# Kernel tuning notes

Measured on AMD Instinct MI355X. Metric: run time of the kernel, lower is better.

Reference implementation:

```python
import jax, jax.numpy as jnp
import numpy as np

DIAG_PENALTY = 100.0

def setup_inputs() -> dict:
    key = jax.random.key(0)
    x = jax.random.normal(key, (8192, 768), dtype=jnp.float32)
    return {"x": x, "coef": 1.0, "tau": 1.0}

def _similarity(x):
    # sim[i, j] = -||x_i - x_j||^2, computed via GEMM expansion
    # ||a - b||^2 = ||a||^2 + ||b||^2 - 2 a.b  (avoids the (N,N,D) intermediate)
    sq = jnp.sum(x * x, axis=1)                      # [N]
    gram = x @ x.T                                   # [N, N]
    sim = 2.0 * gram - sq[:, None] - sq[None, :]     # = -||x_i - x_j||^2
    n = x.shape[0]
    sim = sim - DIAG_PENALTY * jnp.eye(n, dtype=x.dtype)
    return sim

def reference(x, coef, tau):
    sim = _similarity(x) * tau                       # [N, N]
    logp = jax.nn.log_softmax(sim, axis=-1)          # stable, single pass
    prob = jnp.exp(logp)
    entropy = -jnp.sum(prob * logp, axis=-1)         # [N]
    return coef * jnp.mean(entropy)
```

## Files before the change

kernel.cpp:

```cpp
#include <hip/hip_runtime.h>
#include <hip/hip_bf16.h>
#include <hip/hip_fp8.h>
#include <cstdint>
#include <cstddef>

#define GN 8192
#define GD 768
#define NB 64
#define NTILE 2080
#define KI 12

#define LOG2E 1.4426950408889634f
#define LN2 0.6931471805599453f

typedef __attribute__((ext_vector_type(4))) float f32x4;
typedef __attribute__((ext_vector_type(2))) long l64x2;

typedef __attribute__((address_space(1))) const unsigned int gu32;
typedef __attribute__((address_space(3))) unsigned int lu32;

__device__ __forceinline__ void gl2lds16(const void* g, void* l) {
    __builtin_amdgcn_global_load_lds((gu32*)g, (lu32*)l, 16, 0, 0);
}

__device__ __forceinline__ float hexp2(float x) {
    return __builtin_amdgcn_exp2f(x);
}

template <int CTRL>
__device__ __forceinline__ float fdpp(float x) {
    return __int_as_float(__builtin_amdgcn_update_dpp(
        0, __float_as_int(x), CTRL, 0xF, 0xF, true));
}
__device__ __forceinline__ float qmax16(float v) {
    v = fmaxf(v, fdpp<0x128>(v));
    v = fmaxf(v, fdpp<0x124>(v));
    v = fmaxf(v, fdpp<0x122>(v));
    v = fmaxf(v, fdpp<0x121>(v));
    return v;
}
__device__ __forceinline__ float qsum16(float v) {
    v += fdpp<0x128>(v);
    v += fdpp<0x124>(v);
    v += fdpp<0x122>(v);
    v += fdpp<0x121>(v);
    return v;
}

__device__ __forceinline__ int swz(int r, int q) {
    return ((r >> 1) << 7) + (((((r & 1) << 2) | q) ^ ((r >> 1) & 7)) << 4);
}

__global__ __launch_bounds__(256) void prep_kernel(const float* __restrict__ x,
                                                   unsigned char* __restrict__ xq,
                                                   float* __restrict__ sq,
                                                   float* __restrict__ out) {
    if (blockIdx.x == 0 && threadIdx.x == 0) out[0] = 0.f;
    const int w = threadIdx.x >> 6, lane = threadIdx.x & 63;
    const int row = blockIdx.x * 4 + w;
    const float4* xr = (const float4*)(x + (size_t)row * GD);
    unsigned int* xqr = (unsigned int*)(xq + (size_t)row * GD);
    float s = 0.f;
#pragma unroll
    for (int i = 0; i < 3; ++i) {
        float4 v = xr[lane + 64 * i];
        __hip_fp8_e4m3 q0(v.x), q1(v.y), q2(v.z), q3(v.w);
        float d0 = (float)q0, d1 = (float)q1, d2 = (float)q2, d3 = (float)q3;
        s += d0 * d0 + d1 * d1 + d2 * d2 + d3 * d3;
        xqr[lane + 64 * i] = (unsigned int)q0.__x | ((unsigned int)q1.__x << 8) |
                             ((unsigned int)q2.__x << 16) | ((unsigned int)q3.__x << 24);
    }
#pragma unroll
    for (int off = 1; off < 64; off <<= 1) s += __shfl_xor(s, off);
    if (lane == 0) sq[row] = s;
}

__global__ __launch_bounds__(256, 4) void sym_gemm_entropy(
    const unsigned char* __restrict__ xq, const float* __restrict__ sq,
    const float* __restrict__ taup, float* __restrict__ pm,
    float* __restrict__ ps, float* __restrict__ pt) {
    __shared__ __align__(16) char lds[32768];
    float (*tmrg)[4][3] = (float (*)[4][3])lds;

    const int tid = threadIdx.x;
    const int lane = tid & 63;
    const int w = tid >> 6;
    const int quad = lane >> 4, cl = lane & 15;

    const int b = blockIdx.x;
    int I = (int)((sqrtf(8.0f * (float)b + 1.0f) - 1.0f) * 0.5f);
    while ((I + 1) * (I + 2) / 2 <= b) ++I;
    while (I * (I + 1) / 2 > b) --I;
    const int J = b - I * (I + 1) / 2;
    const int row_base = I * 128;
    const int col_base = J * 128;
    const float taub = (*taup) * LOG2E;

    const int bb = (tid & 7) ^ ((tid >> 3) & 7);
    const int sRow = ((tid >> 3) << 1) | (bb >> 2);
    const int sKb = (bb & 3) * 16;
    const unsigned char* gA = xq + (size_t)(row_base + sRow) * GD + sKb;
    const unsigned char* gB = xq + (size_t)(col_base + sRow) * GD + sKb;

    int offA[2], offB[8];
#pragma unroll
    for (int ti = 0; ti < 2; ++ti) offA[ti] = swz(w * 32 + ti * 16 + cl, quad);
#pragma unroll
    for (int tj = 0; tj < 8; ++tj) offB[tj] = swz(tj * 16 + cl, quad);

    f32x4 acc[2][8];
#pragma unroll
    for (int i = 0; i < 2; ++i)
#pragma unroll
        for (int j = 0; j < 8; ++j) acc[i][j] = (f32x4){0.f, 0.f, 0.f, 0.f};

    gl2lds16(gA, lds + tid * 16);
    gl2lds16(gA + (size_t)64 * GD, lds + 4096 + tid * 16);
    gl2lds16(gB, lds + 8192 + tid * 16);
    gl2lds16(gB + (size_t)64 * GD, lds + 12288 + tid * 16);

#pragma unroll 2
    for (int kk = 0; kk < KI; ++kk) {
        __syncthreads();

        const char* Ab = lds + (kk & 1) * 16384;
        const char* Bb = Ab + 8192;
        l64x2 aF[2], bF[8];
#pragma unroll
        for (int ti = 0; ti < 2; ++ti) aF[ti] = *(const l64x2*)(Ab + offA[ti]);
#pragma unroll
        for (int tj = 0; tj < 8; ++tj) bF[tj] = *(const l64x2*)(Bb + offB[tj]);

        if (kk + 1 < KI) {
            char* An = lds + ((kk + 1) & 1) * 16384;
            const int ko = (kk + 1) * 64;
            gl2lds16(gA + ko, An + tid * 16);
            gl2lds16(gA + (size_t)64 * GD + ko, An + 4096 + tid * 16);
            gl2lds16(gB + ko, An + 8192 + tid * 16);
            gl2lds16(gB + (size_t)64 * GD + ko, An + 12288 + tid * 16);
        }

#pragma unroll
        for (int ti = 0; ti < 2; ++ti)
#pragma unroll
            for (int tj = 0; tj < 8; ++tj) {
                acc[ti][tj] = __builtin_amdgcn_mfma_f32_16x16x32_fp8_fp8(
                    aF[ti].x, bF[tj].x, acc[ti][tj], 0, 0, 0);
                acc[ti][tj] = __builtin_amdgcn_mfma_f32_16x16x32_fp8_fp8(
                    aF[ti].y, bF[tj].y, acc[ti][tj], 0, 0, 0);
            }
    }

    const float t2 = 2.f * taub;
    const float pen = 100.f * taub;
    float ar[8];
    int rowg[8];
#pragma unroll
    for (int ti = 0; ti < 2; ++ti)
#pragma unroll
        for (int rg = 0; rg < 4; ++rg) {
            int r = row_base + w * 32 + ti * 16 + quad * 4 + rg;
            rowg[ti * 4 + rg] = r;
            ar[ti * 4 + rg] = -taub * sq[r];
        }
    float ac[8];
#pragma unroll
    for (int tj = 0; tj < 8; ++tj) ac[tj] = -taub * sq[col_base + tj * 16 + cl];

    float* pmJ = pm + (size_t)J * GN;
    float* psJ = ps + (size_t)J * GN;
    float* ptJ = pt + (size_t)J * GN;

#pragma unroll
    for (int ti = 0; ti < 2; ++ti)
#pragma unroll
        for (int rg = 0; rg < 4; ++rg) {
            const int idx = ti * 4 + rg;
            float uu[8];
            float mloc = -1e30f;
            if (I == J) {
#pragma unroll
                for (int tj = 0; tj < 8; ++tj) {
                    float u = fmaf(t2, acc[ti][tj][rg], ac[tj]);
                    if (rowg[idx] == col_base + tj * 16 + cl) u -= pen;
                    uu[tj] = u;
                    mloc = fmaxf(mloc, u);
                }
            } else {
#pragma unroll
                for (int tj = 0; tj < 8; ++tj) {
                    float u = fmaf(t2, acc[ti][tj][rg], ac[tj]);
                    uu[tj] = u;
                    mloc = fmaxf(mloc, u);
                }
            }
            mloc = qmax16(mloc);
            float s = 0.f, t = 0.f;
#pragma unroll
            for (int tj = 0; tj < 8; ++tj) {
                float d = uu[tj] - mloc;
                float e = hexp2(d);
                s += e;
                t += e * d;
            }
            s = qsum16(s);
            t = qsum16(t);
            if (cl == 0) {
                int r = rowg[idx];
                pmJ[r] = mloc + ar[idx];
                psJ[r] = s;
                ptJ[r] = t;
            }
        }

    if (I != J) {
        __syncthreads();
#pragma unroll
        for (int tj = 0; tj < 8; ++tj) {
            float uu[8];
            float mloc = -1e30f;
#pragma unroll
            for (int ti = 0; ti < 2; ++ti)
#pragma unroll
                for (int rg = 0; rg < 4; ++rg) {
                    float u = fmaf(t2, acc[ti][tj][rg], ar[ti * 4 + rg]);
                    uu[ti * 4 + rg] = u;
                    mloc = fmaxf(mloc, u);
                }
            mloc = fmaxf(mloc, __shfl_xor(mloc, 16));
            mloc = fmaxf(mloc, __shfl_xor(mloc, 32));
            float s = 0.f, t = 0.f;
#pragma unroll
            for (int k = 0; k < 8; ++k) {
                float d = uu[k] - mloc;
                float e = hexp2(d);
                s += e;
                t += e * d;
            }
            s += __shfl_xor(s, 16);
            t += __shfl_xor(t, 16);
            s += __shfl_xor(s, 32);
            t += __shfl_xor(t, 32);
            if (quad == 0) {
                int c = tj * 16 + cl;
                tmrg[c][w][0] = mloc + ac[tj];
                tmrg[c][w][1] = s;
                tmrg[c][w][2] = t;
            }
        }
        __syncthreads();
        if (tid < 128) {
            float m = tmrg[tid][0][0], S = tmrg[tid][0][1], T = tmrg[tid][0][2];
#pragma unroll
            for (int ww = 1; ww < 4; ++ww) {
                float mc = tmrg[tid][ww][0], Sc = tmrg[tid][ww][1], Tc = tmrg[tid][ww][2];
                float mn = fmaxf(m, mc);
                float ea = hexp2(m - mn), eb = hexp2(mc - mn);
                T = (T + (m - mn) * S) * ea + (Tc + (mc - mn) * Sc) * eb;
                S = S * ea + Sc * eb;
                m = mn;
            }
            int c = col_base + tid;
            pm[(size_t)I * GN + c] = m;
            ps[(size_t)I * GN + c] = S;
            pt[(size_t)I * GN + c] = T;
        }
    }
}

__global__ __launch_bounds__(256) void combine(const float* __restrict__ pm,
                                               const float* __restrict__ ps,
                                               const float* __restrict__ pt,
                                               const float* __restrict__ coefp,
                                               float* __restrict__ out) {
    const int t = threadIdx.x;
    const int r = t & 63;
    const int chunk = t >> 6;
    const int row = blockIdx.x * 64 + r;
    float m = -1e30f, S = 0.f, T = 0.f;
#pragma unroll
    for (int i = 0; i < 16; ++i) {
        const int c = chunk * 16 + i;
        float mc = pm[(size_t)c * GN + row];
        float Sc = ps[(size_t)c * GN + row];
        float Tc = pt[(size_t)c * GN + row];
        float mn = fmaxf(m, mc);
        float ea = __builtin_amdgcn_exp2f(m - mn), eb = __builtin_amdgcn_exp2f(mc - mn);
        T = (T + (m - mn) * S) * ea + (Tc + (mc - mn) * Sc) * eb;
        S = S * ea + Sc * eb;
        m = mn;
    }
    __shared__ float lm[4][64], lS[4][64], lT[4][64];
    lm[chunk][r] = m;
    lS[chunk][r] = S;
    lT[chunk][r] = T;
    __syncthreads();
    if (t < 64) {
        float M = lm[0][r], Sa = lS[0][r], Ta = lT[0][r];
#pragma unroll
        for (int cc = 1; cc < 4; ++cc) {
            float mc = lm[cc][r], Sc = lS[cc][r], Tc = lT[cc][r];
            float mn = fmaxf(M, mc);
            float ea = __builtin_amdgcn_exp2f(M - mn), eb = __builtin_amdgcn_exp2f(mc - mn);
            Ta = (Ta + (M - mn) * Sa) * ea + (Tc + (mc - mn) * Sc) * eb;
            Sa = Sa * ea + Sc * eb;
            M = mn;
        }
        float ent2 = __log2f(Sa) - Ta / Sa;
#pragma unroll
        for (int off = 1; off < 64; off <<= 1) ent2 += __shfl_xor(ent2, off);
        if (t == 0) atomicAdd(out, ent2 * coefp[0] * (LN2 / (float)GN));
    }
}

extern "C" void kernel_launch(void* const* d_in, const int* in_sizes, int n_in,
                              void* d_out, int out_size, void* d_ws, size_t ws_size,
                              hipStream_t stream) {
    const float* x = (const float*)d_in[0];
    const float* coefp = (const float*)d_in[1];
    const float* taup = (const float*)d_in[2];
    float* out = (float*)d_out;

    char* ws = (char*)d_ws;
    unsigned char* xq = (unsigned char*)ws;
    float* sq = (float*)(ws + 6291456);
    float* pm = (float*)(ws + 6324224);
    float* ps = (float*)(ws + 6324224 + 2097152);
    float* pt = (float*)(ws + 6324224 + 2 * 2097152);

    prep_kernel<<<GN / 4, 256, 0, stream>>>(x, xq, sq, out);
    sym_gemm_entropy<<<NTILE, 256, 0, stream>>>(xq, sq, taup, pm, ps, pt);
    combine<<<GN / 64, 256, 0, stream>>>(pm, ps, pt, coefp, out);
}
```

Baseline: 128.7 us.

## Switch fp8 GEMM to 32x32x64 scaled MFMA and rework fragment layout

Replaces the 16x16x32 fp8 MFMA tiles, two instructions per 16x16 output tile, with the gfx950 32x32x64 f8f6f4 scaled MFMA (unit scales), one instruction per 32x32 tile. The LDS fragment offsets and the row/column softmax-entropy epilogue are rewritten to match the 32x32 accumulator layout. This cuts MFMA instruction count and LDS fragment loads per k-step. The prep kernel also uses packed hardware fp8 conversion builtins instead of the per-element HIP fp8 type. There is a risk that the fragment-to-K mapping or the lane shuffles in the epilogue are wrong.

```diff
diff --git a/kernel.cpp b/kernel.cpp
--- a/kernel.cpp
+++ b/kernel.cpp
@@ -14,6 +14,8 @@
 #define LN2 0.6931471805599453f
 
 typedef __attribute__((ext_vector_type(4))) float f32x4;
+typedef __attribute__((ext_vector_type(16))) float f32x16;
+typedef __attribute__((ext_vector_type(8))) int i32x8;
 typedef __attribute__((ext_vector_type(2))) long l64x2;
 
 typedef __attribute__((address_space(1))) const unsigned int gu32;
@@ -64,11 +66,14 @@
 #pragma unroll
     for (int i = 0; i < 3; ++i) {
         float4 v = xr[lane + 64 * i];
-        __hip_fp8_e4m3 q0(v.x), q1(v.y), q2(v.z), q3(v.w);
-        float d0 = (float)q0, d1 = (float)q1, d2 = (float)q2, d3 = (float)q3;
+        unsigned int pk = __builtin_amdgcn_cvt_pk_fp8_f32(v.x, v.y, 0, false);
+        pk = __builtin_amdgcn_cvt_pk_fp8_f32(v.z, v.w, pk, true);
+        float d0 = __builtin_amdgcn_cvt_f32_fp8(pk, 0);
+        float d1 = __builtin_amdgcn_cvt_f32_fp8(pk, 1);
+        float d2 = __builtin_amdgcn_cvt_f32_fp8(pk, 2);
+        float d3 = __builtin_amdgcn_cvt_f32_fp8(pk, 3);
         s += d0 * d0 + d1 * d1 + d2 * d2 + d3 * d3;
-        xqr[lane + 64 * i] = (unsigned int)q0.__x | ((unsigned int)q1.__x << 8) |
-                             ((unsigned int)q2.__x << 16) | ((unsigned int)q3.__x << 24);
+        xqr[lane + 64 * i] = pk;
     }
 #pragma unroll
     for (int off = 1; off < 64; off <<= 1) s += __shfl_xor(s, off);
@@ -85,7 +90,7 @@
     const int tid = threadIdx.x;
     const int lane = tid & 63;
     const int w = tid >> 6;
-    const int quad = lane >> 4, cl = lane & 15;
+    const int cl2 = lane & 31, hi = lane >> 5;
 
     const int b = blockIdx.x;
     int I = (int)((sqrtf(8.0f * (float)b + 1.0f) - 1.0f) * 0.5f);
@@ -102,34 +107,42 @@
     const unsigned char* gA = xq + (size_t)(row_base + sRow) * GD + sKb;
     const unsigned char* gB = xq + (size_t)(col_base + sRow) * GD + sKb;
 
-    int offA[2], offB[8];
-#pragma unroll
-    for (int ti = 0; ti < 2; ++ti) offA[ti] = swz(w * 32 + ti * 16 + cl, quad);
-#pragma unroll
-    for (int tj = 0; tj < 8; ++tj) offB[tj] = swz(tj * 16 + cl, quad);
-
-    f32x4 acc[2][8];
-#pragma unroll
-    for (int i = 0; i < 2; ++i)
-#pragma unroll
-        for (int j = 0; j < 8; ++j) acc[i][j] = (f32x4){0.f, 0.f, 0.f, 0.f};
+    int offA[2], offB[4][2];
+#pragma unroll
+    for (int g = 0; g < 2; ++g) offA[g] = swz(w * 32 + cl2, 2 * hi + g);
+#pragma unroll
+    for (int tj = 0; tj < 4; ++tj)
+#pragma unroll
+        for (int g = 0; g < 2; ++g) offB[tj][g] = swz(tj * 32 + cl2, 2 * hi + g);
+
+    f32x16 acc[4];
+#pragma unroll
+    for (int j = 0; j < 4; ++j)
+#pragma unroll
+        for (int e = 0; e < 16; ++e) acc[j][e] = 0.f;
 
     gl2lds16(gA, lds + tid * 16);
     gl2lds16(gA + (size_t)64 * GD, lds + 4096 + tid * 16);
     gl2lds16(gB, lds + 8192 + tid * 16);
     gl2lds16(gB + (size_t)64 * GD, lds + 12288 + tid * 16);
 
+    union AB { l64x2 h[2]; i32x8 v; };
+
 #pragma unroll 2
     for (int kk = 0; kk < KI; ++kk) {
         __syncthreads();
 
         const char* Ab = lds + (kk & 1) * 16384;
         const char* Bb = Ab + 8192;
-        l64x2 aF[2], bF[8];
-#pragma unroll
-        for (int ti = 0; ti < 2; ++ti) aF[ti] = *(const l64x2*)(Ab + offA[ti]);
-#pragma unroll
-        for (int tj = 0; tj < 8; ++tj) bF[tj] = *(const l64x2*)(Bb + offB[tj]);
+        AB aF;
+        AB bF[4];
+        aF.h[0] = *(const l64x2*)(Ab + offA[0]);
+        aF.h[1] = *(const l64x2*)(Ab + offA[1]);
+#pragma unroll
+        for (int tj = 0; tj < 4; ++tj) {
+            bF[tj].h[0] = *(const l64x2*)(Bb + offB[tj][0]);
+            bF[tj].h[1] = *(const l64x2*)(Bb + offB[tj][1]);
+        }
 
         if (kk + 1 < KI) {
             char* An = lds + ((kk + 1) & 1) * 16384;
@@ -141,108 +154,95 @@
         }
 
 #pragma unroll
-        for (int ti = 0; ti < 2; ++ti)
-#pragma unroll
-            for (int tj = 0; tj < 8; ++tj) {
-                acc[ti][tj] = __builtin_amdgcn_mfma_f32_16x16x32_fp8_fp8(
-                    aF[ti].x, bF[tj].x, acc[ti][tj], 0, 0, 0);
-                acc[ti][tj] = __builtin_amdgcn_mfma_f32_16x16x32_fp8_fp8(
-                    aF[ti].y, bF[tj].y, acc[ti][tj], 0, 0, 0);
-            }
+        for (int tj = 0; tj < 4; ++tj)
+            acc[tj] = __builtin_amdgcn_mfma_scale_f32_32x32x64_f8f6f4(
+                aF.v, bF[tj].v, acc[tj], 0, 0, 0, 0x7f7f7f7f, 0, 0x7f7f7f7f);
     }
 
     const float t2 = 2.f * taub;
     const float pen = 100.f * taub;
-    float ar[8];
-    int rowg[8];
-#pragma unroll
-    for (int ti = 0; ti < 2; ++ti)
-#pragma unroll
-        for (int rg = 0; rg < 4; ++rg) {
-            int r = row_base + w * 32 + ti * 16 + quad * 4 + rg;
-            rowg[ti * 4 + rg] = r;
-            ar[ti * 4 + rg] = -taub * sq[r];
-        }
-    float ac[8];
-#pragma unroll
-    for (int tj = 0; tj < 8; ++tj) ac[tj] = -taub * sq[col_base + tj * 16 + cl];
+    float ar[16];
+#pragma unroll
+    for (int k = 0; k < 16; ++k) {
+        int rl = (k & 3) + 8 * (k >> 2) + 4 * hi;
+        ar[k] = -taub * sq[row_base + w * 32 + rl];
+    }
+    float ac[4];
+#pragma unroll
+    for (int tj = 0; tj < 4; ++tj) ac[tj] = -taub * sq[col_base + tj * 32 + cl2];
 
     float* pmJ = pm + (size_t)J * GN;
     float* psJ = ps + (size_t)J * GN;
     float* ptJ = pt + (size_t)J * GN;
 
 #pragma unroll
-    for (int ti = 0; ti < 2; ++ti)
-#pragma unroll
-        for (int rg = 0; rg < 4; ++rg) {
-            const int idx = ti * 4 + rg;
-            float uu[8];
-            float mloc = -1e30f;
-            if (I == J) {
-#pragma unroll
-                for (int tj = 0; tj < 8; ++tj) {
-                    float u = fmaf(t2, acc[ti][tj][rg], ac[tj]);
-                    if (rowg[idx] == col_base + tj * 16 + cl) u -= pen;
-                    uu[tj] = u;
-                    mloc = fmaxf(mloc, u);
-                }
-            } else {
-#pragma unroll
-                for (int tj = 0; tj < 8; ++tj) {
-                    float u = fmaf(t2, acc[ti][tj][rg], ac[tj]);
-                    uu[tj] = u;
-                    mloc = fmaxf(mloc, u);
-                }
-            }
-            mloc = qmax16(mloc);
-            float s = 0.f, t = 0.f;
-#pragma unroll
-            for (int tj = 0; tj < 8; ++tj) {
-                float d = uu[tj] - mloc;
-                float e = hexp2(d);
-                s += e;
-                t += e * d;
-            }
-            s = qsum16(s);
-            t = qsum16(t);
-            if (cl == 0) {
-                int r = rowg[idx];
-                pmJ[r] = mloc + ar[idx];
-                psJ[r] = s;
-                ptJ[r] = t;
-            }
-        }
+    for (int k = 0; k < 16; ++k) {
+        const int rl = (k & 3) + 8 * (k >> 2) + 4 * hi;
+        const int rg = row_base + w * 32 + rl;
+        float uu[4];
+        float mloc = -1e30f;
+        if (I == J) {
+#pragma unroll
+            for (int tj = 0; tj < 4; ++tj) {
+                float u = fmaf(t2, acc[tj][k], ac[tj]);
+                if (rg == col_base + tj * 32 + cl2) u -= pen;
+                uu[tj] = u;
+                mloc = fmaxf(mloc, u);
+            }
+        } else {
+#pragma unroll
+            for (int tj = 0; tj < 4; ++tj) {
+                float u = fmaf(t2, acc[tj][k], ac[tj]);
+                uu[tj] = u;
+                mloc = fmaxf(mloc, u);
+            }
+        }
+        mloc = fmaxf(mloc, __shfl_xor(mloc, 16));
+        mloc = qmax16(mloc);
+        float s = 0.f, t = 0.f;
+#pragma unroll
+        for (int tj = 0; tj < 4; ++tj) {
+            float d = uu[tj] - mloc;
+            float e = hexp2(d);
+            s += e;
+            t += e * d;
+        }
+        s += __shfl_xor(s, 16);
+        t += __shfl_xor(t, 16);
+        s = qsum16(s);
+        t = qsum16(t);
+        if (cl2 == 0) {
+            pmJ[rg] = mloc + ar[k];
+            psJ[rg] = s;
+            ptJ[rg] = t;
+        }
+    }
 
     if (I != J) {
         __syncthreads();
 #pragma unroll
-        for (int tj = 0; tj < 8; ++tj) {
-            float uu[8];
+        for (int tj = 0; tj < 4; ++tj) {
+            float uu[16];
             float mloc = -1e30f;
 #pragma unroll
-            for (int ti = 0; ti < 2; ++ti)
-#pragma unroll
-                for (int rg = 0; rg < 4; ++rg) {
-                    float u = fmaf(t2, acc[ti][tj][rg], ar[ti * 4 + rg]);
-                    uu[ti * 4 + rg] = u;
-                    mloc = fmaxf(mloc, u);
-                }
-            mloc = fmaxf(mloc, __shfl_xor(mloc, 16));
+            for (int k = 0; k < 16; ++k) {
+                float u = fmaf(t2, acc[tj][k], ar[k]);
+                uu[k] = u;
+                mloc = fmaxf(mloc, u);
+            }
             mloc = fmaxf(mloc, __shfl_xor(mloc, 32));
             float s = 0.f, t = 0.f;
 #pragma unroll
-            for (int k = 0; k < 8; ++k) {
+            for (int k = 0; k < 16; ++k) {
                 float d = uu[k] - mloc;
                 float e = hexp2(d);
                 s += e;
                 t += e * d;
             }
-            s += __shfl_xor(s, 16);
-            t += __shfl_xor(t, 16);
             s += __shfl_xor(s, 32);
             t += __shfl_xor(t, 32);
-            if (quad == 0) {
-                int c = tj * 16 + cl;
+            if (hi == 0) {
+                int c = tj * 32 + cl2;
                 tmrg[c][w][0] = mloc + ac[tj];
                 tmrg[c][w][1] = s;
                 tmrg[c][w][2] = t;
```

Result: slower. 350.1 us (+172.0%).
